# Performance work log

Measured on AMD Instinct MI355X. Metric: run time of the kernel, lower is better.

Reference implementation:

```python
import jax, jax.numpy as jnp
import numpy as np


def setup_inputs() -> dict:
    key = jax.random.key(0)
    k1, k2 = jax.random.split(key)
    B, C_in, H, Wd = 8, 64, 64, 64
    C_a = 32
    x = jax.random.normal(k1, (B, C_in, H, Wd), dtype=jnp.float32)
    # 1x1 conv == per-pixel linear map: weight [C_a, C_in], bias [C_a]
    W = jax.random.normal(k2, (C_a, C_in), dtype=jnp.float32) * (1.0 / np.sqrt(C_in))
    b = jnp.zeros((C_a,), dtype=jnp.float32)
    return {"x": x, "W": W, "b": b}


def reference(x, W, b):
    B, C, H, Wd = x.shape
    N = H * Wd
    # g = 1x1 conv: [B, C_a, H, W] -> flatten spatial -> [B, C_a, N]
    g = jnp.einsum('oc,bchw->bohw', W, x) + b[None, :, None, None]
    g = g.reshape(B, -1, N)
    # alpha[b, n, m] = softmax_m( sum_c g[b,c,n] * g[b,c,m] )  (unscaled)
    scores = jnp.einsum('bcn,bcm->bnm', g, g)
    alpha = jax.nn.softmax(scores, axis=2)
    # r[b, c, n] = sum_m alpha[b,n,m] * x[b,c,m]
    xf = x.reshape(B, C, N)
    r = jnp.einsum('bnm,bcm->bcn', alpha, xf)
    # residual (intended semantics of is_residual=True) + ReLU epilogue
    r = r + xf
    out = jax.nn.relu(r).reshape(B, C, H, Wd)
    return (out, alpha)
```

## Files before the change

kernel.cpp:

```cpp
#include <hip/hip_runtime.h>
#include <math.h>

#define BB 8
#define CC 64
#define NA 4096
#define KA 32
#define LOG2E 1.4426950408889634f

typedef short bfrag __attribute__((ext_vector_type(8)));
typedef int   i4    __attribute__((ext_vector_type(4)));
typedef float f4    __attribute__((ext_vector_type(4)));
typedef float f16v  __attribute__((ext_vector_type(16)));

__device__ __forceinline__ f16v mf(bfrag a, bfrag b, f16v c) {
    return __builtin_amdgcn_mfma_f32_32x32x16_bf16(a, b, c, 0, 0, 0);
}

__device__ __forceinline__ unsigned short bfrne(float f) {
    unsigned u = __builtin_bit_cast(unsigned, f);
    return (unsigned short)((u + 0x7FFFu + ((u >> 16) & 1u)) >> 16);
}
__device__ __forceinline__ unsigned pk2(float a, float b) {
    return (unsigned)bfrne(a) | ((unsigned)bfrne(b) << 16);
}
__device__ __forceinline__ float bf2f(unsigned short h) {
    unsigned u = ((unsigned)h) << 16;
    return __builtin_bit_cast(float, u);
}

__global__ __launch_bounds__(256) void k_g(const float* __restrict__ x,
                                           const float* __restrict__ W,
                                           const float* __restrict__ bias,
                                           short* __restrict__ ghi,
                                           short* __restrict__ glo,
                                           float* __restrict__ norms,
                                           int* __restrict__ gmaxi,
                                           float* __restrict__ lsum) {
    __shared__ float Wl[KA * CC];
    __shared__ float bl[KA];
    __shared__ float red[4];
    int tid = threadIdx.x;
    for (int i = tid; i < KA * CC; i += 256) Wl[i] = W[i];
    if (tid < KA) bl[tid] = bias[tid];
    __syncthreads();

    int b = blockIdx.y;
    int n = blockIdx.x * 256 + tid;

    float acc[KA];
#pragma unroll
    for (int k = 0; k < KA; k++) acc[k] = 0.f;

    const float* xp = x + (size_t)b * CC * NA + n;
#pragma unroll 4
    for (int c = 0; c < CC; c++) {
        float xv = xp[(size_t)c * NA];
#pragma unroll
        for (int k = 0; k < KA; k++) acc[k] = fmaf(Wl[k * CC + c], xv, acc[k]);
    }

    float ss = 0.f;
    unsigned ph[KA / 2], pl[KA / 2];
#pragma unroll
    for (int k = 0; k < KA; k += 2) {
        float v0 = acc[k] + bl[k];
        float v1 = acc[k + 1] + bl[k + 1];
        ss = fmaf(v0, v0, fmaf(v1, v1, ss));
        unsigned short h0 = bfrne(v0), h1 = bfrne(v1);
        float l0 = v0 - bf2f(h0), l1 = v1 - bf2f(h1);
        ph[k / 2] = (unsigned)h0 | ((unsigned)h1 << 16);
        pl[k / 2] = (unsigned)bfrne(l0) | ((unsigned)bfrne(l1) << 16);
    }
    float nrm = sqrtf(ss);
    norms[b * NA + n] = nrm;
    lsum[b * NA + n] = 0.f;

    size_t row = ((size_t)b * NA + n) * KA;
#pragma unroll
    for (int q = 0; q < 4; q++) {
        i4 vh = { (int)ph[4 * q], (int)ph[4 * q + 1], (int)ph[4 * q + 2], (int)ph[4 * q + 3] };
        i4 vl = { (int)pl[4 * q], (int)pl[4 * q + 1], (int)pl[4 * q + 2], (int)pl[4 * q + 3] };
        *(i4*)(ghi + row + q * 8) = vh;
        *(i4*)(glo + row + q * 8) = vl;
    }

    float m = nrm;
#pragma unroll
    for (int off = 1; off < 64; off <<= 1) m = fmaxf(m, __shfl_xor(m, off));
    if ((tid & 63) == 0) red[tid >> 6] = m;
    __syncthreads();
    if (tid == 0) {
        float bm = fmaxf(fmaxf(red[0], red[1]), fmaxf(red[2], red[3]));
        atomicMax(&gmaxi[b], __float_as_int(bm));
    }
}

__global__ __launch_bounds__(256) void k_xb(const float* __restrict__ x,
                                            short* __restrict__ xb2) {
    __shared__ float t[64][65];
    const int tid = threadIdx.x;
    const int b = blockIdx.y;
    const int m0 = blockIdx.x * 64;

    const int c0 = tid >> 4, m4 = (tid & 15) * 4;
#pragma unroll
    for (int p = 0; p < 4; p++) {
        int c = p * 16 + c0;
        f4 v = *(const f4*)(x + ((size_t)b * CC + c) * NA + m0 + m4);
        t[c][m4 + 0] = v[0];
        t[c][m4 + 1] = v[1];
        t[c][m4 + 2] = v[2];
        t[c][m4 + 3] = v[3];
    }
    __syncthreads();

    short* xo = xb2 + (size_t)b * CC * NA;
#pragma unroll
    for (int q = 0; q < 2; q++) {
        int idx = q * 256 + tid;
        int mgl = idx >> 6, c = idx & 63;
        i4 pkd;
#pragma unroll
        for (int j = 0; j < 4; j++)
            pkd[j] = (int)pk2(t[c][mgl * 8 + 2 * j], t[c][mgl * 8 + 2 * j + 1]);
        *(i4*)(xo + (size_t)(((m0 >> 3) + mgl) * 64 + c) * 8) = pkd;
    }
}

__global__ __launch_bounds__(256, 4) void k_den(const short* __restrict__ ghi,
                                                const short* __restrict__ glo,
                                                const float* __restrict__ norms,
                                                const int* __restrict__ gmaxi,
                                                float* __restrict__ lsum) {
    __shared__ float rowsum[4][32];
    const int tid = threadIdx.x;
    const int w = tid >> 6;
    const int l31 = tid & 31;
    const int hi = (tid >> 5) & 1;
    const int id = blockIdx.x;
    const int b = id & 7;
    const int rr = id >> 3;
    const int nb = rr & 127;
    const int mc = rr >> 7;
    const int n0 = nb * 32;

    const float gmax = __int_as_float(gmaxi[b]);
    const float C2 = -norms[b * NA + n0 + l31] * gmax * LOG2E;
    const short* gh = ghi + (size_t)b * NA * KA;
    const short* gl = glo + (size_t)b * NA * KA;

    bfrag Bh[2], Bl[2];
#pragma unroll
    for (int kt = 0; kt < 2; kt++) {
        size_t o = (size_t)(n0 + l31) * KA + kt * 16 + hi * 8;
        Bh[kt] = *(const bfrag*)(gh + o);
        Bl[kt] = *(const bfrag*)(gl + o);
    }

    float ls = 0.f;
#pragma unroll 2
    for (int i = 0; i < 8; i++) {
        const int m0 = (mc * 8 + i) * 128 + w * 32;
        bfrag Ah[2], Al[2];
#pragma unroll
        for (int kt = 0; kt < 2; kt++) {
            size_t o = (size_t)(m0 + l31) * KA + kt * 16 + hi * 8;
            Ah[kt] = *(const bfrag*)(gh + o);
            Al[kt] = *(const bfrag*)(gl + o);
        }
        f16v sA = {}, sB = {};
        sA = mf(Ah[0], Bh[0], sA); sA = mf(Ah[1], Bh[1], sA);
        sB = mf(Ah[0], Bl[0], sB); sB = mf(Ah[1], Bl[1], sB);
        sB = mf(Al[0], Bh[0], sB); sB = mf(Al[1], Bh[1], sB);
#pragma unroll
        for (int r = 0; r < 16; r++) ls += exp2f(fmaf(sA[r] + sB[r], LOG2E, C2));
    }
    ls += __shfl_xor(ls, 32);
    if (hi == 0) rowsum[w][l31] = ls;
    __syncthreads();
    if (tid < 32)
        atomicAdd(&lsum[b * NA + n0 + tid],
                  rowsum[0][tid] + rowsum[1][tid] + rowsum[2][tid] + rowsum[3][tid]);
}

#define LOADA(dst, m0v) do { \
    size_t _o = (size_t)((m0v) + l31) * KA + hi * 8; \
    dst[0] = *(const bfrag*)(gh + _o); \
    dst[1] = *(const bfrag*)(gh + _o + 16); \
    dst[2] = *(const bfrag*)(gl + _o); \
    dst[3] = *(const bfrag*)(gl + _o + 16); } while (0)

#define LOADX(dst, m0v) do { \
    const int _mg = (m0v) >> 3; \
    dst[0] = *(const bfrag*)(xp + (size_t)((_mg + hi) * 64 + l31) * 8); \
    dst[1] = *(const bfrag*)(xp + (size_t)((_mg + 2 + hi) * 64 + l31) * 8); \
    dst[2] = *(const bfrag*)(xp + (size_t)((_mg + hi) * 64 + 32 + l31) * 8); \
    dst[3] = *(const bfrag*)(xp + (size_t)((_mg + 2 + hi) * 64 + 32 + l31) * 8); } while (0)

__global__ __launch_bounds__(256, 2) void k_attn2(const float* __restrict__ x,
                                                  const short* __restrict__ ghi,
                                                  const short* __restrict__ glo,
                                                  const short* __restrict__ xb2,
                                                  const float* __restrict__ norms,
                                                  const int* __restrict__ gmaxi,
                                                  const float* __restrict__ lsum,
                                                  float* __restrict__ out,
                                                  float* __restrict__ alpha) {
    __shared__ __align__(16) char smem[2 * 32 * 256 * 4];
    float* ast = (float*)smem;

    const int tid = threadIdx.x;
    const int w = tid >> 6;
    const int l = tid & 63;
    const int l31 = tid & 31;
    const int hi = (tid >> 5) & 1;
    const int id = blockIdx.x;
    const int b = id & 7;
    const int n0 = (id >> 3) * 32;

    const float M = norms[b * NA + n0 + l31] * __int_as_float(gmaxi[b]);
    const float C2L = fmaf(-M, LOG2E, -__log2f(lsum[b * NA + n0 + l31]));

    const short* gh = ghi + (size_t)b * NA * KA;
    const short* gl = glo + (size_t)b * NA * KA;
    const short* xp = xb2 + (size_t)b * CC * NA;
    float* ap = alpha + (size_t)b * NA * NA;

    bfrag Bh[2], Bl[2];
#pragma unroll
    for (int kt = 0; kt < 2; kt++) {
        size_t o = (size_t)(n0 + l31) * KA + kt * 16 + hi * 8;
        Bh[kt] = *(const bfrag*)(gh + o);
        Bl[kt] = *(const bfrag*)(gl + o);
    }

    f16v pv0 = {}, pv1 = {};

    bfrag Af0[4], Af1[4], Xf0[4], Xf1[4];
    LOADA(Af0, w * 32);
    LOADX(Xf0, w * 32);

    for (int it = 0; it < 16; ++it) {
        float* astb = ast + (it & 1) * 8192;
        const int mb = it * 256 + w * 32;

        LOADA(Af1, mb + 128);
        LOADX(Xf1, mb + 128);
        {
            f16v sA = {}, sB = {};
            sA = mf(Af0[0], Bh[0], sA); sA = mf(Af0[1], Bh[1], sA);
            sB = mf(Af0[0], Bl[0], sB); sB = mf(Af0[1], Bl[1], sB);
            sB = mf(Af0[2], Bh[0], sB); sB = mf(Af0[3], Bh[1], sB);

            float a[16];
#pragma unroll
            for (int r = 0; r < 16; r++) a[r] = exp2f(fmaf(sA[r] + sB[r], LOG2E, C2L));

#pragma unroll
            for (int q = 0; q < 4; q++) {
                f4 v = { a[4 * q], a[4 * q + 1], a[4 * q + 2], a[4 * q + 3] };
                int phys = (w * 8 + 2 * q + hi) ^ (l31 & 7);
                *(f4*)&astb[l31 * 256 + phys * 4] = v;
            }

            unsigned p0 = pk2(a[0], a[1]),   p1 = pk2(a[2], a[3]);
            unsigned p2 = pk2(a[4], a[5]),   p3 = pk2(a[6], a[7]);
            unsigned p4 = pk2(a[8], a[9]),   p5 = pk2(a[10], a[11]);
            unsigned p6 = pk2(a[12], a[13]), p7 = pk2(a[14], a[15]);
            asm("v_permlane32_swap_b32 %0, %1" : "+v"(p0), "+v"(p2));
            asm("v_permlane32_swap_b32 %0, %1" : "+v"(p1), "+v"(p3));
            asm("v_permlane32_swap_b32 %0, %1" : "+v"(p4), "+v"(p6));
            asm("v_permlane32_swap_b32 %0, %1" : "+v"(p5), "+v"(p7));
            i4 f0 = { (int)p0, (int)p1, (int)p2, (int)p3 };
            i4 f1 = { (int)p4, (int)p5, (int)p6, (int)p7 };
            bfrag pa0 = __builtin_bit_cast(bfrag, f0);
            bfrag pa1 = __builtin_bit_cast(bfrag, f1);

            pv0 = mf(pa0, Xf0[0], pv0); pv0 = mf(pa1, Xf0[1], pv0);
            pv1 = mf(pa0, Xf0[2], pv1); pv1 = mf(pa1, Xf0[3], pv1);
        }

        if (it < 15) {
            LOADA(Af0, mb + 256);
            LOADX(Xf0, mb + 256);
        }
        {
            f16v sA = {}, sB = {};
            sA = mf(Af1[0], Bh[0], sA); sA = mf(Af1[1], Bh[1], sA);
            sB = mf(Af1[0], Bl[0], sB); sB = mf(Af1[1], Bl[1], sB);
            sB = mf(Af1[2], Bh[0], sB); sB = mf(Af1[3], Bh[1], sB);

            float a[16];
#pragma unroll
            for (int r = 0; r < 16; r++) a[r] = exp2f(fmaf(sA[r] + sB[r], LOG2E, C2L));

#pragma unroll
            for (int q = 0; q < 4; q++) {
                f4 v = { a[4 * q], a[4 * q + 1], a[4 * q + 2], a[4 * q + 3] };
                int phys = (w * 8 + 2 * q + hi) ^ (l31 & 7);
                *(f4*)&astb[l31 * 256 + 128 + phys * 4] = v;
            }

            unsigned p0 = pk2(a[0], a[1]),   p1 = pk2(a[2], a[3]);
            unsigned p2 = pk2(a[4], a[5]),   p3 = pk2(a[6], a[7]);
            unsigned p4 = pk2(a[8], a[9]),   p5 = pk2(a[10], a[11]);
            unsigned p6 = pk2(a[12], a[13]), p7 = pk2(a[14], a[15]);
            asm("v_permlane32_swap_b32 %0, %1" : "+v"(p0), "+v"(p2));
            asm("v_permlane32_swap_b32 %0, %1" : "+v"(p1), "+v"(p3));
            asm("v_permlane32_swap_b32 %0, %1" : "+v"(p4), "+v"(p6));
            asm("v_permlane32_swap_b32 %0, %1" : "+v"(p5), "+v"(p7));
            i4 f0 = { (int)p0, (int)p1, (int)p2, (int)p3 };
            i4 f1 = { (int)p4, (int)p5, (int)p6, (int)p7 };
            bfrag pa0 = __builtin_bit_cast(bfrag, f0);
            bfrag pa1 = __builtin_bit_cast(bfrag, f1);

            pv0 = mf(pa0, Xf1[0], pv0); pv0 = mf(pa1, Xf1[1], pv0);
            pv1 = mf(pa0, Xf1[2], pv1); pv1 = mf(pa1, Xf1[3], pv1);
        }

        asm volatile("s_waitcnt lgkmcnt(0)\n\ts_barrier" ::: "memory");

#pragma unroll
        for (int e = 0; e < 8; e++) {
            int row = w * 8 + e;
            int c4 = l;
            int phys = (c4 & 31) ^ e;
            f4 v = *(const f4*)&astb[row * 256 + (c4 >> 5) * 128 + phys * 4];
            __builtin_nontemporal_store(v, (f4*)(ap + (size_t)(n0 + row) * NA + it * 256 + c4 * 4));
        }
    }
    __syncthreads();

    float (*pvr0)[CC + 1] = (float(*)[CC + 1])smem;
    float (*pvr1)[CC + 1] = (float(*)[CC + 1])(smem + 32 * (CC + 1) * 4);
    if (w >= 2) {
        float (*buf)[CC + 1] = (w == 2) ? pvr0 : pvr1;
#pragma unroll
        for (int r = 0; r < 16; r++) {
            int nl = (r & 3) + 8 * (r >> 2) + 4 * hi;
            buf[nl][l31]      = pv0[r];
            buf[nl][32 + l31] = pv1[r];
        }
    }
    __syncthreads();
    if (w < 2) {
        float (*buf)[CC + 1] = (w == 0) ? pvr0 : pvr1;
#pragma unroll
        for (int r = 0; r < 16; r++) {
            int nl = (r & 3) + 8 * (r >> 2) + 4 * hi;
            buf[nl][l31]      += pv0[r];
            buf[nl][32 + l31] += pv1[r];
        }
    }
    __syncthreads();

    const float* xr = x + (size_t)b * CC * NA + n0;
    float* op = out + (size_t)b * CC * NA + n0;
#pragma unroll
    for (int e = 0; e < 8; e++) {
        int idx = e * 256 + tid;
        int c = idx >> 5, n = idx & 31;
        float v = pvr0[n][c] + pvr1[n][c] + xr[(size_t)c * NA + n];
        op[(size_t)c * NA + n] = fmaxf(v, 0.f);
    }
}

extern "C" void kernel_launch(void* const* d_in, const int* in_sizes, int n_in,
                              void* d_out, int out_size, void* d_ws, size_t ws_size,
                              hipStream_t stream) {
    const float* x = (const float*)d_in[0];
    const float* W = (const float*)d_in[1];
    const float* bias = (const float*)d_in[2];

    float* out = (float*)d_out;
    float* alpha = out + (size_t)BB * CC * NA;

    short* ghi = (short*)d_ws;
    short* glo = ghi + (size_t)BB * NA * KA;
    short* xb2 = glo + (size_t)BB * NA * KA;
    float* norms = (float*)(xb2 + (size_t)BB * CC * NA);
    int*   gmaxi = (int*)(norms + (size_t)BB * NA);
    float* lsum  = (float*)(gmaxi + 8);

    k_g<<<dim3(NA / 256, BB), 256, 0, stream>>>(x, W, bias, ghi, glo, norms, gmaxi, lsum);
    k_xb<<<dim3(NA / 64, BB), 256, 0, stream>>>(x, xb2);
    k_den<<<4096, 256, 0, stream>>>(ghi, glo, norms, gmaxi, lsum);
    k_attn2<<<1024, 256, 0, stream>>>(x, ghi, glo, xb2, norms, gmaxi, lsum, out, alpha);
}
```

Baseline: 180.9 us.

## Fuse bf16 x repack into k_g, use hardware bf16 pack, drop nontemporal stores

Removes the separate k_xb kernel. k_g now writes the bf16-rounded x values into shared memory while it computes g, then stores them in the blocked xb2 layout, which saves one launch and one re-read of x. In k_attn2 the software round-to-nearest pack is replaced with the v_cvt_pk_bf16_f32 instruction, cutting VALU work in the inner loop. The alpha stores change from nontemporal to ordinary stores, which may change cache behaviour for the large alpha write. The fused path adds about 33KB of LDS to k_g and relies on its existing barrier before the read-back.

```diff
diff --git a/kernel.cpp b/kernel.cpp
--- a/kernel.cpp
+++ b/kernel.cpp
@@ -20,12 +20,14 @@
     unsigned u = __builtin_bit_cast(unsigned, f);
     return (unsigned short)((u + 0x7FFFu + ((u >> 16) & 1u)) >> 16);
 }
-__device__ __forceinline__ unsigned pk2(float a, float b) {
-    return (unsigned)bfrne(a) | ((unsigned)bfrne(b) << 16);
-}
 __device__ __forceinline__ float bf2f(unsigned short h) {
     unsigned u = ((unsigned)h) << 16;
     return __builtin_bit_cast(float, u);
+}
+__device__ __forceinline__ unsigned cvtpk(float a, float b) {
+    unsigned r;
+    asm("v_cvt_pk_bf16_f32 %0, %1, %2" : "=v"(r) : "v"(a), "v"(b));
+    return r;
 }
 
 __global__ __launch_bounds__(256) void k_g(const float* __restrict__ x,
@@ -35,10 +37,12 @@
                                            short* __restrict__ glo,
                                            float* __restrict__ norms,
                                            int* __restrict__ gmaxi,
-                                           float* __restrict__ lsum) {
+                                           float* __restrict__ lsum,
+                                           short* __restrict__ xb2) {
     __shared__ float Wl[KA * CC];
     __shared__ float bl[KA];
     __shared__ float red[4];
+    __shared__ short lx[CC][264];
     int tid = threadIdx.x;
     for (int i = tid; i < KA * CC; i += 256) Wl[i] = W[i];
     if (tid < KA) bl[tid] = bias[tid];
@@ -55,6 +59,7 @@
 #pragma unroll 4
     for (int c = 0; c < CC; c++) {
         float xv = xp[(size_t)c * NA];
+        lx[c][tid] = (short)bfrne(xv);
 #pragma unroll
         for (int k = 0; k < KA; k++) acc[k] = fmaf(Wl[k * CC + c], xv, acc[k]);
     }
@@ -93,37 +98,15 @@
         float bm = fmaxf(fmaxf(red[0], red[1]), fmaxf(red[2], red[3]));
         atomicMax(&gmaxi[b], __float_as_int(bm));
     }
-}
-
-__global__ __launch_bounds__(256) void k_xb(const float* __restrict__ x,
-                                            short* __restrict__ xb2) {
-    __shared__ float t[64][65];
-    const int tid = threadIdx.x;
-    const int b = blockIdx.y;
-    const int m0 = blockIdx.x * 64;
-
-    const int c0 = tid >> 4, m4 = (tid & 15) * 4;
-#pragma unroll
-    for (int p = 0; p < 4; p++) {
-        int c = p * 16 + c0;
-        f4 v = *(const f4*)(x + ((size_t)b * CC + c) * NA + m0 + m4);
-        t[c][m4 + 0] = v[0];
-        t[c][m4 + 1] = v[1];
-        t[c][m4 + 2] = v[2];
-        t[c][m4 + 3] = v[3];
-    }
-    __syncthreads();
 
     short* xo = xb2 + (size_t)b * CC * NA;
-#pragma unroll
-    for (int q = 0; q < 2; q++) {
+    const int mg0 = blockIdx.x * 32;
+#pragma unroll
+    for (int q = 0; q < 8; q++) {
         int idx = q * 256 + tid;
         int mgl = idx >> 6, c = idx & 63;
-        i4 pkd;
-#pragma unroll
-        for (int j = 0; j < 4; j++)
-            pkd[j] = (int)pk2(t[c][mgl * 8 + 2 * j], t[c][mgl * 8 + 2 * j + 1]);
-        *(i4*)(xo + (size_t)(((m0 >> 3) + mgl) * 64 + c) * 8) = pkd;
+        i4 v = *(const i4*)&lx[c][mgl * 8];
+        *(i4*)(xo + (size_t)((mg0 + mgl) * 64 + c) * 8) = v;
     }
 }
 
@@ -263,10 +246,10 @@
                 *(f4*)&astb[l31 * 256 + phys * 4] = v;
             }
 
-            unsigned p0 = pk2(a[0], a[1]),   p1 = pk2(a[2], a[3]);
-            unsigned p2 = pk2(a[4], a[5]),   p3 = pk2(a[6], a[7]);
-            unsigned p4 = pk2(a[8], a[9]),   p5 = pk2(a[10], a[11]);
-            unsigned p6 = pk2(a[12], a[13]), p7 = pk2(a[14], a[15]);
+            unsigned p0 = cvtpk(a[0], a[1]),   p1 = cvtpk(a[2], a[3]);
+            unsigned p2 = cvtpk(a[4], a[5]),   p3 = cvtpk(a[6], a[7]);
+            unsigned p4 = cvtpk(a[8], a[9]),   p5 = cvtpk(a[10], a[11]);
+            unsigned p6 = cvtpk(a[12], a[13]), p7 = cvtpk(a[14], a[15]);
             asm("v_permlane32_swap_b32 %0, %1" : "+v"(p0), "+v"(p2));
             asm("v_permlane32_swap_b32 %0, %1" : "+v"(p1), "+v"(p3));
             asm("v_permlane32_swap_b32 %0, %1" : "+v"(p4), "+v"(p6));
@@ -301,10 +284,10 @@
                 *(f4*)&astb[l31 * 256 + 128 + phys * 4] = v;
             }
 
-            unsigned p0 = pk2(a[0], a[1]),   p1 = pk2(a[2], a[3]);
-            unsigned p2 = pk2(a[4], a[5]),   p3 = pk2(a[6], a[7]);
-            unsigned p4 = pk2(a[8], a[9]),   p5 = pk2(a[10], a[11]);
-            unsigned p6 = pk2(a[12], a[13]), p7 = pk2(a[14], a[15]);
+            unsigned p0 = cvtpk(a[0], a[1]),   p1 = cvtpk(a[2], a[3]);
+            unsigned p2 = cvtpk(a[4], a[5]),   p3 = cvtpk(a[6], a[7]);
+            unsigned p4 = cvtpk(a[8], a[9]),   p5 = cvtpk(a[10], a[11]);
+            unsigned p6 = cvtpk(a[12], a[13]), p7 = cvtpk(a[14], a[15]);
             asm("v_permlane32_swap_b32 %0, %1" : "+v"(p0), "+v"(p2));
             asm("v_permlane32_swap_b32 %0, %1" : "+v"(p1), "+v"(p3));
             asm("v_permlane32_swap_b32 %0, %1" : "+v"(p4), "+v"(p6));
@@ -326,7 +309,7 @@
             int c4 = l;
             int phys = (c4 & 31) ^ e;
             f4 v = *(const f4*)&astb[row * 256 + (c4 >> 5) * 128 + phys * 4];
-            __builtin_nontemporal_store(v, (f4*)(ap + (size_t)(n0 + row) * NA + it * 256 + c4 * 4));
+            *(f4*)(ap + (size_t)(n0 + row) * NA + it * 256 + c4 * 4) = v;
         }
     }
     __syncthreads();
@@ -382,8 +365,7 @@
     int*   gmaxi = (int*)(norms + (size_t)BB * NA);
     float* lsum  = (float*)(gmaxi + 8);
 
-    k_g<<<dim3(NA / 256, BB), 256, 0, stream>>>(x, W, bias, ghi, glo, norms, gmaxi, lsum);
-    k_xb<<<dim3(NA / 64, BB), 256, 0, stream>>>(x, xb2);
+    k_g<<<dim3(NA / 256, BB), 256, 0, stream>>>(x, W, bias, ghi, glo, norms, gmaxi, lsum, xb2);
     k_den<<<4096, 256, 0, stream>>>(ghi, glo, norms, gmaxi, lsum);
     k_attn2<<<1024, 256, 0, stream>>>(x, ghi, glo, xb2, norms, gmaxi, lsum, out, alpha);
 }
```

Measured after the change: 209.8 us. +16.0%, slower.
